# Optimization experiments

Hardware: AMD Instinct MI355X
Metric: run time of the kernel (lower is better)

## Reference

```python
import jax, jax.numpy as jnp
import numpy as np

B, Q, K = 16, 8192, 8192
D_QK, D_V = 64, 64      # raw query/key and value feature dims
H = 8                    # num_heads
DP = 128                 # proj_qks output dim (per default MLP [128, 128])
VP = 64                  # proj_vs output dim (per default MLP [128, 64])
LN_EPS = 1e-6            # flax LayerNorm default


def setup_inputs() -> dict:
    key = jax.random.key(0)
    ks_ = jax.random.split(key, 12)
    f = lambda k, s: jax.random.normal(k, s, jnp.float32)
    return {
        "qs": f(ks_[0], (B, Q, D_QK)),
        "ks": f(ks_[1], (B, K, D_QK)),
        "vs": f(ks_[2], (B, K, D_V)),
        "qs_s": f(ks_[3], (B, Q, D_QK)),
        "ks_s": f(ks_[4], (B, K, D_QK)),
        "valid_lens": jax.random.randint(ks_[5], (B,), 1, K + 1, jnp.int32),
        # proj_qks = MLP([128, 128], gelu): Dense(128) -> gelu -> Dense(128)
        "Wq1": f(ks_[6], (2 * D_QK, DP)) / np.sqrt(2 * D_QK).astype(np.float32),
        "bq1": jnp.zeros((DP,), jnp.float32),
        "Wq2": f(ks_[7], (DP, DP)) / np.sqrt(DP).astype(np.float32),
        "bq2": jnp.zeros((DP,), jnp.float32),
        # proj_vs = MLP([128, 64], gelu): Dense(128) -> gelu -> Dense(64)
        "Wv1": f(ks_[8], (D_V, DP)) / np.sqrt(D_V).astype(np.float32),
        "bv1": jnp.zeros((DP,), jnp.float32),
        "Wv2": f(ks_[9], (DP, VP)) / np.sqrt(DP).astype(np.float32),
        "bv2": jnp.zeros((VP,), jnp.float32),
        "ln_scale": jnp.ones((VP,), jnp.float32),
        "ln_bias": jnp.zeros((VP,), jnp.float32),
    }


def _mlp2(x, W1, b1, W2, b2):
    # Dense -> gelu (tanh approx, flax default) -> Dense
    return jax.nn.gelu(x @ W1 + b1) @ W2 + b2


def reference(qs, ks, vs, qs_s, ks_s, valid_lens,
              Wq1, bq1, Wq2, bq2, Wv1, bv1, Wv2, bv2,
              ln_scale, ln_bias):
    Kl, D = ks.shape[-2], ks.shape[-1]  # D taken BEFORE stacking, as in source
    scale = D ** 0.25
    # stack spatial features then feature-map MLPs
    q = _mlp2(jnp.concatenate([qs_s, qs], axis=-1), Wq1, bq1, Wq2, bq2) / scale
    k = _mlp2(jnp.concatenate([ks_s, ks], axis=-1), Wq1, bq1, Wq2, bq2) / scale
    v = _mlp2(vs, Wv1, bv1, Wv2, bv2)
    # valid-length masking of keys, mean-style normalization of values
    mask = (jnp.arange(Kl)[None, :] < valid_lens[:, None]).astype(k.dtype)[..., None]
    k = k * mask
    v = v / valid_lens[:, None, None].astype(v.dtype)
    Bn, Qn = q.shape[0], q.shape[1]
    q = q.reshape(Bn, Qn, H, DP // H)   # B Q H d
    k = k.reshape(Bn, Kl, H, DP // H)   # B K H d
    v = v.reshape(Bn, Kl, H, VP // H)   # B K H e
    # linear attention: KV outer-product summary then apply queries
    kv = jnp.einsum('bkhd,bkhe->bhde', k, v)          # B H d e
    ctx = jnp.einsum('bqhd,bhde->bqhe', q, kv)        # B Q H e
    ctx = ctx.reshape(Bn, Qn, VP)
    # LayerNorm over last dim
    mu = ctx.mean(-1, keepdims=True)
    var = ((ctx - mu) ** 2).mean(-1, keepdims=True)
    return (ctx - mu) * jax.lax.rsqrt(var + LN_EPS) * ln_scale + ln_bias
```

## Files before the change

### kernel.cpp

```cpp
#include <hip/hip_runtime.h>
#include <hip/hip_bf16.h>


typedef __attribute__((ext_vector_type(8))) short short8;
typedef __attribute__((ext_vector_type(4))) float f32x4;
typedef unsigned int u32;
typedef unsigned short u16;

#define MFMA(A,B,C) __builtin_amdgcn_mfma_f32_16x16x32_bf16((A),(B),(C),0,0,0)
#define SBAR() __builtin_amdgcn_sched_barrier(0)

#define LDH 136
#define LDT 40
#define INVS 0.3535533905932738f

__device__ __forceinline__ u16 bfc(float x){
  __hip_bfloat16 h = __float2bfloat16(x);
  return __bfloat16_as_ushort(h);
}
__device__ __forceinline__ u32 pack2(float a, float b){
  return (u32)bfc(a) | ((u32)bfc(b) << 16);
}
__device__ __forceinline__ float b2f(u16 w){
  return __uint_as_float(((u32)w) << 16);
}
__device__ __forceinline__ short8 cvt8(f32x4 lo, f32x4 hi){
  short8 r;
  r[0]=(short)bfc(lo[0]); r[1]=(short)bfc(lo[1]);
  r[2]=(short)bfc(lo[2]); r[3]=(short)bfc(lo[3]);
  r[4]=(short)bfc(hi[0]); r[5]=(short)bfc(hi[1]);
  r[6]=(short)bfc(hi[2]); r[7]=(short)bfc(hi[3]);
  return r;
}
__device__ __forceinline__ float gelu_f(float x){
  float s = x*x;
  float u = x * __builtin_fmaf(s, 0.035677408136300125f, 0.7978845608028654f);
  float e = __builtin_amdgcn_exp2f(u * -2.885390081777927f);
  return x * __builtin_amdgcn_rcpf(1.0f + e);
}

__global__ void dk_prep(const float* __restrict__ Wq1, const float* __restrict__ Wq2,
                        const float* __restrict__ Wv1, const float* __restrict__ Wv2,
                        u16* __restrict__ wt){
  int i = blockIdx.x*256 + threadIdx.x;
  int e = i & 7;
  int lane = (i >> 3) & 63;
  int chunk = i >> 9;
  int c = lane & 15, g = lane >> 4;
  int k0 = 8*g + e;
  float v;
  if (chunk < 32){
    int mt = chunk >> 2, ks4 = chunk & 3;
    v = Wq1[(ks4*32 + k0)*128 + mt*16 + c];
  } else if (chunk < 64){
    int ch = chunk - 32; int mt = ch >> 2, ks4 = ch & 3;
    v = Wq2[(ks4*32 + k0)*128 + mt*16 + c] * INVS;
  } else if (chunk < 80){
    int ch = chunk - 64; int mt = ch >> 1, ks2 = ch & 1;
    v = Wv1[(ks2*32 + k0)*128 + mt*16 + c];
  } else {
    int ch = chunk - 80; int n2 = ch >> 2, ks4 = ch & 3;
    v = Wv2[(ks4*32 + k0)*64 + n2*16 + c];
  }
  wt[i] = bfc(v);
}

__global__ __launch_bounds__(128, 2) void dk_stage1(
    const float* __restrict__ ksp, const float* __restrict__ kssp,
    const float* __restrict__ vsp, const int* __restrict__ vlen,
    const float* __restrict__ bq1, const float* __restrict__ bq2,
    const float* __restrict__ bv1, const float* __restrict__ bv2,
    const u16* __restrict__ wt, float* __restrict__ kvgr, int repmask)
{
  __shared__ u16 sA[2][5120];
  __shared__ u16 sB[2][2560];
  const int tid = threadIdx.x;
  const int w = tid >> 6, l = tid & 63;
  const int c = l & 15, g = l >> 4;

  int pfx = (l < 16) ? ((vlen[l] + 63) >> 6) : 0;
  #pragma unroll
  for (int m=1; m<16; m<<=1){
    int v = __shfl_up(pfx, m, 64);
    if (l >= m) pfx += v;
  }
  const int T = __shfl(pfx, 15, 64);
  const int t = blockIdx.x;
  if (t >= T) return;
  unsigned long long mk = __ballot(l < 16 && pfx <= t);
  const int b = __popcll(mk);
  const int jb = t - (b ? __shfl(pfx, b-1, 64) : 0);
  const int len = vlen[b];
  const int rbase = jb*64 + w*32;
  if (rbase >= len) return;
  const int rep = t & repmask;
  const size_t row0 = (size_t)b*8192 + rbase;

  u16* H1 = sA[w];
  u16* KT = sA[w];
  u16* VT = sB[w];
  const u16* Wq1t = wt;
  const u16* Wq2t = wt + 16384;
  const u16* Wv1t = wt + 32768;
  const u16* Wv2t = wt + 40960;
  const f32x4 z4 = {0.f,0.f,0.f,0.f};

  {
    f32x4 xvf[8];
    #pragma unroll
    for (int ks2=0; ks2<2; ++ks2){
      #pragma unroll
      for (int nt=0; nt<2; ++nt){
        const float* src = vsp + (row0 + nt*16 + c)*64 + ks2*32 + 8*g;
        xvf[(ks2*2+nt)*2+0] = *(const f32x4*)src;
        xvf[(ks2*2+nt)*2+1] = *(const f32x4*)(src+4);
      }
    }
    SBAR();
    short8 xv[2][2];
    #pragma unroll
    for (int ks2=0; ks2<2; ++ks2)
      #pragma unroll
      for (int nt=0; nt<2; ++nt)
        xv[ks2][nt] = cvt8(xvf[(ks2*2+nt)*2+0], xvf[(ks2*2+nt)*2+1]);
    f32x4 av[8][2];
    #pragma unroll
    for (int mt=0; mt<8; ++mt){ av[mt][0]=z4; av[mt][1]=z4; }
    #pragma unroll
    for (int ks2=0; ks2<2; ++ks2){
      short8 wa[8];
      #pragma unroll
      for (int mt=0; mt<8; ++mt)
        wa[mt] = *(const short8*)&Wv1t[((mt*2+ks2)*64 + l)*8];
      SBAR();
      #pragma unroll
      for (int mt=0; mt<8; ++mt){
        av[mt][0] = MFMA(wa[mt], xv[ks2][0], av[mt][0]);
        av[mt][1] = MFMA(wa[mt], xv[ks2][1], av[mt][1]);
      }
    }
    #pragma unroll
    for (int mt=0; mt<8; ++mt){
      const f32x4 bia = *(const f32x4*)&bv1[mt*16 + 4*g];
      #pragma unroll
      for (int nt=0; nt<2; ++nt){
        uint2 pp;
        pp.x = pack2(gelu_f(av[mt][nt][0]+bia[0]), gelu_f(av[mt][nt][1]+bia[1]));
        pp.y = pack2(gelu_f(av[mt][nt][2]+bia[2]), gelu_f(av[mt][nt][3]+bia[3]));
        *(uint2*)&H1[(nt*16 + c)*LDH + mt*16 + 4*g] = pp;
      }
    }
  }
  {
    f32x4 acv[2][4];
    #pragma unroll
    for (int n2=0; n2<4; ++n2){ acv[0][n2]=z4; acv[1][n2]=z4; }
    #pragma unroll
    for (int ks4=0; ks4<4; ++ks4){
      short8 wb[4];
      #pragma unroll
      for (int n2=0; n2<4; ++n2)
        wb[n2] = *(const short8*)&Wv2t[((n2*4+ks4)*64 + l)*8];
      SBAR();
      const short8 ah0 = *(const short8*)&H1[(c     )*LDH + ks4*32 + 8*g];
      const short8 ah1 = *(const short8*)&H1[(16 + c)*LDH + ks4*32 + 8*g];
      #pragma unroll
      for (int n2=0; n2<4; ++n2){
        acv[0][n2] = MFMA(ah0, wb[n2], acv[0][n2]);
        acv[1][n2] = MFMA(ah1, wb[n2], acv[1][n2]);
      }
    }
    #pragma unroll
    for (int n2=0; n2<4; ++n2){
      const float bb = bv2[n2*16 + c];
      #pragma unroll
      for (int mt=0; mt<2; ++mt){
        uint2 pp;
        pp.x = pack2(acv[mt][n2][0]+bb, acv[mt][n2][1]+bb);
        pp.y = pack2(acv[mt][n2][2]+bb, acv[mt][n2][3]+bb);
        *(uint2*)&VT[(n2*16+c)*LDT + mt*16 + 4*g] = pp;
      }
    }
  }
  {
    f32x4 xkf[16];
    #pragma unroll
    for (int ks4=0; ks4<4; ++ks4){
      #pragma unroll
      for (int nt=0; nt<2; ++nt){
        const int kk = ks4*32 + 8*g;
        const float* src = (ks4 < 2) ? (kssp + (row0 + nt*16 + c)*64 + kk)
                                     : (ksp  + (row0 + nt*16 + c)*64 + (kk - 64));
        xkf[(ks4*2+nt)*2+0] = *(const f32x4*)src;
        xkf[(ks4*2+nt)*2+1] = *(const f32x4*)(src+4);
      }
    }
    SBAR();
    short8 xk[4][2];
    #pragma unroll
    for (int ks4=0; ks4<4; ++ks4)
      #pragma unroll
      for (int nt=0; nt<2; ++nt)
        xk[ks4][nt] = cvt8(xkf[(ks4*2+nt)*2+0], xkf[(ks4*2+nt)*2+1]);
    f32x4 acc[8][2];
    #pragma unroll
    for (int mt=0; mt<8; ++mt){ acc[mt][0]=z4; acc[mt][1]=z4; }
    #pragma unroll
    for (int ks4=0; ks4<4; ++ks4){
      short8 wa[8];
      #pragma unroll
      for (int mt=0; mt<8; ++mt)
        wa[mt] = *(const short8*)&Wq1t[((mt*4+ks4)*64 + l)*8];
      SBAR();
      #pragma unroll
      for (int mt=0; mt<8; ++mt){
        acc[mt][0] = MFMA(wa[mt], xk[ks4][0], acc[mt][0]);
        acc[mt][1] = MFMA(wa[mt], xk[ks4][1], acc[mt][1]);
      }
    }
    #pragma unroll
    for (int mt=0; mt<8; ++mt){
      const f32x4 bia = *(const f32x4*)&bq1[mt*16 + 4*g];
      #pragma unroll
      for (int nt=0; nt<2; ++nt){
        uint2 pp;
        pp.x = pack2(gelu_f(acc[mt][nt][0]+bia[0]), gelu_f(acc[mt][nt][1]+bia[1]));
        pp.y = pack2(gelu_f(acc[mt][nt][2]+bia[2]), gelu_f(acc[mt][nt][3]+bia[3]));
        *(uint2*)&H1[(nt*16 + c)*LDH + mt*16 + 4*g] = pp;
      }
    }
  }
  {
    f32x4 acc2[2][8];
    #pragma unroll
    for (int n2=0; n2<8; ++n2){ acc2[0][n2]=z4; acc2[1][n2]=z4; }
    #pragma unroll
    for (int ks4=0; ks4<4; ++ks4){
      short8 wb[8];
      #pragma unroll
      for (int n2=0; n2<8; ++n2)
        wb[n2] = *(const short8*)&Wq2t[((n2*4+ks4)*64 + l)*8];
      SBAR();
      const short8 ah0 = *(const short8*)&H1[(c     )*LDH + ks4*32 + 8*g];
      const short8 ah1 = *(const short8*)&H1[(16 + c)*LDH + ks4*32 + 8*g];
      #pragma unroll
      for (int n2=0; n2<8; ++n2){
        acc2[0][n2] = MFMA(ah0, wb[n2], acc2[0][n2]);
        acc2[1][n2] = MFMA(ah1, wb[n2], acc2[1][n2]);
      }
    }
    #pragma unroll
    for (int n2=0; n2<8; ++n2){
      const float bb = bq2[n2*16 + c] * INVS;
      #pragma unroll
      for (int mt=0; mt<2; ++mt){
        const int r0 = rbase + mt*16 + 4*g;
        float v0 = (r0+0 < len) ? acc2[mt][n2][0] + bb : 0.f;
        float v1 = (r0+1 < len) ? acc2[mt][n2][1] + bb : 0.f;
        float v2 = (r0+2 < len) ? acc2[mt][n2][2] + bb : 0.f;
        float v3 = (r0+3 < len) ? acc2[mt][n2][3] + bb : 0.f;
        uint2 pp; pp.x = pack2(v0,v1); pp.y = pack2(v2,v3);
        *(uint2*)&KT[(n2*16 + c)*LDT + mt*16 + 4*g] = pp;
      }
    }
  }
  {
    short8 zf = {0,0,0,0,0,0,0,0};
    f32x4 kvacc[8];
    #pragma unroll
    for (int h=0; h<8; ++h) kvacc[h] = z4;
    #pragma unroll
    for (int h=0; h<8; ++h){
      const short8 ka = *(const short8*)&KT[(h*16 + c)*LDT + 8*g];
      short8 vb = zf;
      if (c < 8) vb = *(const short8*)&VT[(h*8 + c)*LDT + 8*g];
      kvacc[h] = MFMA(ka, vb, kvacc[h]);
    }
    if (c < 8){
      float* kvg = kvgr + ((size_t)rep*16 + b)*1024;
      #pragma unroll
      for (int h=0; h<8; ++h){
        #pragma unroll
        for (int r=0; r<4; ++r)
          atomicAdd(&kvg[(h*16 + 4*g + r)*8 + c], kvacc[h][r]);
      }
    }
  }
}

__global__ void dk_mid(const float* __restrict__ kvgr, int nrep,
                       const int* __restrict__ vlen,
                       const float* __restrict__ bq2,
                       const u16* __restrict__ wt,
                       u16* __restrict__ Mt, float* __restrict__ c0g)
{
  __shared__ float kvs[1024];
  const int b = blockIdx.x, t = threadIdx.x;
  const float inv_len = 1.0f / (float)vlen[b];
  #pragma unroll
  for (int k=0; k<4; ++k){
    const int idx = t + 256*k;
    float s = 0.f;
    for (int r=0; r<nrep; ++r) s += kvgr[((size_t)r*16 + b)*1024 + idx];
    kvs[idx] = s * inv_len;
  }
  __syncthreads();
  for (int k=0; k<32; ++k){
    const int o = t + 256*k;
    const int e = o >> 7, j = o & 127;
    const int h = e >> 3, e8 = e & 7;
    const int ks4 = j >> 5, gg = (j >> 3) & 3, el = j & 7;
    float s = 0.f;
    #pragma unroll
    for (int d=0; d<16; ++d){
      const int od = h*16 + d;
      const u16 wv = wt[16384 + (((od>>4)*4 + ks4)*64 + gg*16 + (od&15))*8 + el];
      s += b2f(wv) * kvs[h*128 + d*8 + e8];
    }
    const int n3 = e >> 4, cc = e & 15;
    Mt[(size_t)b*8192 + ((n3*4 + ks4)*64 + gg*16 + cc)*8 + el] = bfc(s);
  }
  if (t < 64){
    const int e = t, h = e >> 3, e8 = e & 7;
    float s = 0.f;
    #pragma unroll
    for (int d=0; d<16; ++d)
      s += bq2[h*16+d] * INVS * kvs[h*128 + d*8 + e8];
    c0g[b*64 + e] = s;
  }
}

__global__ __launch_bounds__(128, 2) void dk_stage2(
    const float* __restrict__ qsp, const float* __restrict__ qssp,
    const float* __restrict__ bq1,
    const float* __restrict__ lnw_g, const float* __restrict__ lnb_g,
    const u16* __restrict__ wt, const u16* __restrict__ Mt,
    const float* __restrict__ c0g, float* __restrict__ outp)
{
  __shared__ u16 sH1[2][32*LDH];
  const int tid = threadIdx.x;
  const int w = tid >> 6, l = tid & 63;
  const int c = l & 15, g = l >> 4;
  const int b  = blockIdx.x >> 7;
  const int jb = blockIdx.x & 127;
  const int rbase = jb*64 + w*32;
  u16* H1 = sH1[w];
  const u16* Wq1t = wt;
  const size_t row0 = (size_t)b*8192 + rbase;
  const f32x4 z4 = {0.f,0.f,0.f,0.f};

  {
    f32x4 xqf[16];
    #pragma unroll
    for (int ks4=0; ks4<4; ++ks4){
      #pragma unroll
      for (int nt=0; nt<2; ++nt){
        const int kk = ks4*32 + 8*g;
        const float* src = (ks4 < 2) ? (qssp + (row0 + nt*16 + c)*64 + kk)
                                     : (qsp  + (row0 + nt*16 + c)*64 + (kk - 64));
        xqf[(ks4*2+nt)*2+0] = *(const f32x4*)src;
        xqf[(ks4*2+nt)*2+1] = *(const f32x4*)(src+4);
      }
    }
    SBAR();
    short8 xq[4][2];
    #pragma unroll
    for (int ks4=0; ks4<4; ++ks4)
      #pragma unroll
      for (int nt=0; nt<2; ++nt)
        xq[ks4][nt] = cvt8(xqf[(ks4*2+nt)*2+0], xqf[(ks4*2+nt)*2+1]);
    f32x4 acc[8][2];
    #pragma unroll
    for (int mt=0; mt<8; ++mt){ acc[mt][0]=z4; acc[mt][1]=z4; }
    #pragma unroll
    for (int ks4=0; ks4<4; ++ks4){
      short8 wa[8];
      #pragma unroll
      for (int mt=0; mt<8; ++mt)
        wa[mt] = *(const short8*)&Wq1t[((mt*4+ks4)*64 + l)*8];
      SBAR();
      #pragma unroll
      for (int mt=0; mt<8; ++mt){
        acc[mt][0] = MFMA(wa[mt], xq[ks4][0], acc[mt][0]);
        acc[mt][1] = MFMA(wa[mt], xq[ks4][1], acc[mt][1]);
      }
    }
    #pragma unroll
    for (int mt=0; mt<8; ++mt){
      const f32x4 bia = *(const f32x4*)&bq1[mt*16 + 4*g];
      #pragma unroll
      for (int nt=0; nt<2; ++nt){
        uint2 pp;
        pp.x = pack2(gelu_f(acc[mt][nt][0]+bia[0]), gelu_f(acc[mt][nt][1]+bia[1]));
        pp.y = pack2(gelu_f(acc[mt][nt][2]+bia[2]), gelu_f(acc[mt][nt][3]+bia[3]));
        *(uint2*)&H1[(nt*16 + c)*LDH + mt*16 + 4*g] = pp;
      }
    }
  }
  f32x4 acc3[2][4];
  #pragma unroll
  for (int n3=0; n3<4; ++n3){ acc3[0][n3]=z4; acc3[1][n3]=z4; }
  const u16* Mb = Mt + (size_t)b*8192;
  {
    short8 bm[16];
    #pragma unroll
    for (int ks4=0; ks4<4; ++ks4)
      #pragma unroll
      for (int n3=0; n3<4; ++n3)
        bm[ks4*4+n3] = *(const short8*)&Mb[((n3*4+ks4)*64 + l)*8];
    SBAR();
    #pragma unroll
    for (int ks4=0; ks4<4; ++ks4){
      const short8 aq0 = *(const short8*)&H1[(c     )*LDH + ks4*32 + 8*g];
      const short8 aq1 = *(const short8*)&H1[(16 + c)*LDH + ks4*32 + 8*g];
      #pragma unroll
      for (int n3=0; n3<4; ++n3){
        acc3[0][n3] = MFMA(aq0, bm[ks4*4+n3], acc3[0][n3]);
        acc3[1][n3] = MFMA(aq1, bm[ks4*4+n3], acc3[1][n3]);
      }
    }
  }
  float c0v[4];
  #pragma unroll
  for (int n3=0; n3<4; ++n3) c0v[n3] = c0g[b*64 + n3*16 + c];
  float lnw[4], lnb[4];
  #pragma unroll
  for (int n3=0; n3<4; ++n3){ lnw[n3] = lnw_g[n3*16 + c]; lnb[n3] = lnb_g[n3*16 + c]; }
  float* Tb = (float*)H1;
  #pragma unroll
  for (int mt=0; mt<2; ++mt){
    #pragma unroll
    for (int r=0; r<4; ++r){
      float s1 = 0.f, s2 = 0.f;
      #pragma unroll
      for (int n3=0; n3<4; ++n3){
        float v = acc3[mt][n3][r] + c0v[n3];
        s1 += v; s2 += v*v;
      }
      #pragma unroll
      for (int m=1; m<16; m<<=1){
        s1 += __shfl_xor(s1, m, 64);
        s2 += __shfl_xor(s2, m, 64);
      }
      const float mu = s1 * (1.0f/64.0f);
      const float var = s2 * (1.0f/64.0f) - mu*mu;
      const float rs = rsqrtf(var + 1e-6f);
      const int rloc = mt*16 + 4*g + r;
      #pragma unroll
      for (int n3=0; n3<4; ++n3)
        Tb[rloc*68 + n3*16 + c] = (acc3[mt][n3][r] + c0v[n3] - mu)*rs*lnw[n3] + lnb[n3];
    }
  }
  float* ob = outp + row0*64;
  #pragma unroll
  for (int i=0; i<8; ++i){
    const int row = i*4 + (l>>4);
    const f32x4 vv = *(const f32x4*)&Tb[row*68 + (l&15)*4];
    *(f32x4*)(ob + row*64 + (l&15)*4) = vv;
  }
}

extern "C" void kernel_launch(void* const* d_in, const int* in_sizes, int n_in,
                              void* d_out, int out_size, void* d_ws, size_t ws_size,
                              hipStream_t stream)
{
  const float* qs   = (const float*)d_in[0];
  const float* ks   = (const float*)d_in[1];
  const float* vs   = (const float*)d_in[2];
  const float* qs_s = (const float*)d_in[3];
  const float* ks_s = (const float*)d_in[4];
  const int*   vl   = (const int*)d_in[5];
  const float* Wq1  = (const float*)d_in[6];
  const float* bq1  = (const float*)d_in[7];
  const float* Wq2  = (const float*)d_in[8];
  const float* bq2  = (const float*)d_in[9];
  const float* Wv1  = (const float*)d_in[10];
  const float* bv1  = (const float*)d_in[11];
  const float* Wv2  = (const float*)d_in[12];
  const float* bv2  = (const float*)d_in[13];
  const float* lnw  = (const float*)d_in[14];
  const float* lnb  = (const float*)d_in[15];
  (void)in_sizes; (void)n_in; (void)out_size;

  const size_t fixed = 96*1024 + 256*1024 + 4096;
  int nrep = 4;
  while (nrep > 1 && (size_t)nrep*65536 + fixed > ws_size) nrep >>= 1;
  float* kvgr = (float*)d_ws;
  u16*   wt   = (u16*)((char*)d_ws + (size_t)nrep*65536);
  u16*   Mt   = (u16*)((char*)wt + 96*1024);
  float* c0   = (float*)((char*)Mt + 256*1024);

  hipMemsetAsync(kvgr, 0, (size_t)nrep*65536, stream);
  dk_prep<<<192, 256, 0, stream>>>(Wq1, Wq2, Wv1, Wv2, wt);
  dk_stage1<<<2048, 128, 0, stream>>>(ks, ks_s, vs, vl, bq1, bq2, bv1, bv2,
                                      wt, kvgr, nrep - 1);
  dk_mid<<<16, 256, 0, stream>>>(kvgr, nrep, vl, bq2, wt, Mt, c0);
  dk_stage2<<<2048, 128, 0, stream>>>(qs, qs_s, bq1, lnw, lnb, wt, Mt, c0,
                                      (float*)d_out);
}
```

Baseline: 92.17 us.

## Halve rows per wave to 16 and double grid with higher occupancy

Each wave now processes 16 rows instead of 32 in both stage kernels, halving accumulator arrays, input register buffers and LDS buffers, while doubling the grid to 4096 blocks and raising launch bounds to 4 blocks per SIMD. The KV outer-product MFMA now uses a K-dimension of 16 by zeroing the upper lane groups. The aim is more resident waves to hide global-load latency. In exchange, each weight fragment loaded from global/L2 is reused over half as many rows, so weight traffic per row doubles, and half the KV MFMA work is wasted on zeros.

```diff
diff --git a/kernel.cpp b/kernel.cpp
--- a/kernel.cpp
+++ b/kernel.cpp
@@ -11,7 +11,7 @@
 #define SBAR() __builtin_amdgcn_sched_barrier(0)
 
 #define LDH 136
-#define LDT 40
+#define LDT 24
 #define INVS 0.3535533905932738f
 
 __device__ __forceinline__ u16 bfc(float x){
@@ -65,20 +65,20 @@
   wt[i] = bfc(v);
 }
 
-__global__ __launch_bounds__(128, 2) void dk_stage1(
+__global__ __launch_bounds__(128, 4) void dk_stage1(
     const float* __restrict__ ksp, const float* __restrict__ kssp,
     const float* __restrict__ vsp, const int* __restrict__ vlen,
     const float* __restrict__ bq1, const float* __restrict__ bq2,
     const float* __restrict__ bv1, const float* __restrict__ bv2,
     const u16* __restrict__ wt, float* __restrict__ kvgr, int repmask)
 {
-  __shared__ u16 sA[2][5120];
-  __shared__ u16 sB[2][2560];
+  __shared__ u16 sA[2][3072];
+  __shared__ u16 sB[2][1536];
   const int tid = threadIdx.x;
   const int w = tid >> 6, l = tid & 63;
   const int c = l & 15, g = l >> 4;
 
-  int pfx = (l < 16) ? ((vlen[l] + 63) >> 6) : 0;
+  int pfx = (l < 16) ? ((vlen[l] + 31) >> 5) : 0;
   #pragma unroll
   for (int m=1; m<16; m<<=1){
     int v = __shfl_up(pfx, m, 64);
@@ -91,7 +91,7 @@
   const int b = __popcll(mk);
   const int jb = t - (b ? __shfl(pfx, b-1, 64) : 0);
   const int len = vlen[b];
-  const int rbase = jb*64 + w*32;
+  const int rbase = jb*32 + w*16;
   if (rbase >= len) return;
   const int rep = t & repmask;
   const size_t row0 = (size_t)b*8192 + rbase;
@@ -104,28 +104,24 @@
   const u16* Wv1t = wt + 32768;
   const u16* Wv2t = wt + 40960;
   const f32x4 z4 = {0.f,0.f,0.f,0.f};
-
-  {
-    f32x4 xvf[8];
+  const short8 zf = {0,0,0,0,0,0,0,0};
+
+  {
+    f32x4 xvf[4];
     #pragma unroll
     for (int ks2=0; ks2<2; ++ks2){
-      #pragma unroll
-      for (int nt=0; nt<2; ++nt){
-        const float* src = vsp + (row0 + nt*16 + c)*64 + ks2*32 + 8*g;
-        xvf[(ks2*2+nt)*2+0] = *(const f32x4*)src;
-        xvf[(ks2*2+nt)*2+1] = *(const f32x4*)(src+4);
-      }
+      const float* src = vsp + (row0 + c)*64 + ks2*32 + 8*g;
+      xvf[ks2*2+0] = *(const f32x4*)src;
+      xvf[ks2*2+1] = *(const f32x4*)(src+4);
     }
     SBAR();
-    short8 xv[2][2];
+    short8 xv[2];
     #pragma unroll
     for (int ks2=0; ks2<2; ++ks2)
-      #pragma unroll
-      for (int nt=0; nt<2; ++nt)
-        xv[ks2][nt] = cvt8(xvf[(ks2*2+nt)*2+0], xvf[(ks2*2+nt)*2+1]);
-    f32x4 av[8][2];
-    #pragma unroll
-    for (int mt=0; mt<8; ++mt){ av[mt][0]=z4; av[mt][1]=z4; }
+      xv[ks2] = cvt8(xvf[ks2*2+0], xvf[ks2*2+1]);
+    f32x4 av[8];
+    #pragma unroll
+    for (int mt=0; mt<8; ++mt) av[mt] = z4;
     #pragma unroll
     for (int ks2=0; ks2<2; ++ks2){
       short8 wa[8];
@@ -134,27 +130,22 @@
         wa[mt] = *(const short8*)&Wv1t[((mt*2+ks2)*64 + l)*8];
       SBAR();
       #pragma unroll
-      for (int mt=0; mt<8; ++mt){
-        av[mt][0] = MFMA(wa[mt], xv[ks2][0], av[mt][0]);
-        av[mt][1] = MFMA(wa[mt], xv[ks2][1], av[mt][1]);
-      }
+      for (int mt=0; mt<8; ++mt)
+        av[mt] = MFMA(wa[mt], xv[ks2], av[mt]);
     }
     #pragma unroll
     for (int mt=0; mt<8; ++mt){
       const f32x4 bia = *(const f32x4*)&bv1[mt*16 + 4*g];
-      #pragma unroll
-      for (int nt=0; nt<2; ++nt){
-        uint2 pp;
-        pp.x = pack2(gelu_f(av[mt][nt][0]+bia[0]), gelu_f(av[mt][nt][1]+bia[1]));
-        pp.y = pack2(gelu_f(av[mt][nt][2]+bia[2]), gelu_f(av[mt][nt][3]+bia[3]));
-        *(uint2*)&H1[(nt*16 + c)*LDH + mt*16 + 4*g] = pp;
-      }
-    }
-  }
-  {
-    f32x4 acv[2][4];
-    #pragma unroll
-    for (int n2=0; n2<4; ++n2){ acv[0][n2]=z4; acv[1][n2]=z4; }
+      uint2 pp;
+      pp.x = pack2(gelu_f(av[mt][0]+bia[0]), gelu_f(av[mt][1]+bia[1]));
+      pp.y = pack2(gelu_f(av[mt][2]+bia[2]), gelu_f(av[mt][3]+bia[3]));
+      *(uint2*)&H1[c*LDH + mt*16 + 4*g] = pp;
+    }
+  }
+  {
+    f32x4 acv[4];
+    #pragma unroll
+    for (int n2=0; n2<4; ++n2) acv[n2] = z4;
     #pragma unroll
     for (int ks4=0; ks4<4; ++ks4){
       short8 wb[4];
@@ -162,49 +153,38 @@
       for (int n2=0; n2<4; ++n2)
         wb[n2] = *(const short8*)&Wv2t[((n2*4+ks4)*64 + l)*8];
       SBAR();
-      const short8 ah0 = *(const short8*)&H1[(c     )*LDH + ks4*32 + 8*g];
-      const short8 ah1 = *(const short8*)&H1[(16 + c)*LDH + ks4*32 + 8*g];
-      #pragma unroll
-      for (int n2=0; n2<4; ++n2){
-        acv[0][n2] = MFMA(ah0, wb[n2], acv[0][n2]);
-        acv[1][n2] = MFMA(ah1, wb[n2], acv[1][n2]);
-      }
+      const short8 ah = *(const short8*)&H1[c*LDH + ks4*32 + 8*g];
+      #pragma unroll
+      for (int n2=0; n2<4; ++n2)
+        acv[n2] = MFMA(ah, wb[n2], acv[n2]);
     }
     #pragma unroll
     for (int n2=0; n2<4; ++n2){
       const float bb = bv2[n2*16 + c];
-      #pragma unroll
-      for (int mt=0; mt<2; ++mt){
-        uint2 pp;
-        pp.x = pack2(acv[mt][n2][0]+bb, acv[mt][n2][1]+bb);
-        pp.y = pack2(acv[mt][n2][2]+bb, acv[mt][n2][3]+bb);
-        *(uint2*)&VT[(n2*16+c)*LDT + mt*16 + 4*g] = pp;
-      }
-    }
-  }
-  {
-    f32x4 xkf[16];
-    #pragma unroll
-    for (int ks4=0; ks4<4; ++ks4){
-      #pragma unroll
-      for (int nt=0; nt<2; ++nt){
-        const int kk = ks4*32 + 8*g;
-        const float* src = (ks4 < 2) ? (kssp + (row0 + nt*16 + c)*64 + kk)
-                                     : (ksp  + (row0 + nt*16 + c)*64 + (kk - 64));
-        xkf[(ks4*2+nt)*2+0] = *(const f32x4*)src;
-        xkf[(ks4*2+nt)*2+1] = *(const f32x4*)(src+4);
-      }
+      uint2 pp;
+      pp.x = pack2(acv[n2][0]+bb, acv[n2][1]+bb);
+      pp.y = pack2(acv[n2][2]+bb, acv[n2][3]+bb);
+      *(uint2*)&VT[(n2*16+c)*LDT + 4*g] = pp;
+    }
+  }
+  {
+    f32x4 xkf[8];
+    #pragma unroll
+    for (int ks4=0; ks4<4; ++ks4){
+      const int kk = ks4*32 + 8*g;
+      const float* src = (ks4 < 2) ? (kssp + (row0 + c)*64 + kk)
+                                   : (ksp  + (row0 + c)*64 + (kk - 64));
+      xkf[ks4*2+0] = *(const f32x4*)src;
+      xkf[ks4*2+1] = *(const f32x4*)(src+4);
     }
     SBAR();
-    short8 xk[4][2];
+    short8 xk[4];
     #pragma unroll
     for (int ks4=0; ks4<4; ++ks4)
-      #pragma unroll
-      for (int nt=0; nt<2; ++nt)
-        xk[ks4][nt] = cvt8(xkf[(ks4*2+nt)*2+0], xkf[(ks4*2+nt)*2+1]);
-    f32x4 acc[8][2];
-    #pragma unroll
-    for (int mt=0; mt<8; ++mt){ acc[mt][0]=z4; acc[mt][1]=z4; }
+      xk[ks4] = cvt8(xkf[ks4*2+0], xkf[ks4*2+1]);
+    f32x4 acc[8];
+    #pragma unroll
+    for (int mt=0; mt<8; ++mt) acc[mt] = z4;
     #pragma unroll
     for (int ks4=0; ks4<4; ++ks4){
       short8 wa[8];
@@ -213,27 +193,22 @@
         wa[mt] = *(const short8*)&Wq1t[((mt*4+ks4)*64 + l)*8];
       SBAR();
       #pragma unroll
-      for (int mt=0; mt<8; ++mt){
-        acc[mt][0] = MFMA(wa[mt], xk[ks4][0], acc[mt][0]);
-        acc[mt][1] = MFMA(wa[mt], xk[ks4][1], acc[mt][1]);
-      }
+      for (int mt=0; mt<8; ++mt)
+        acc[mt] = MFMA(wa[mt], xk[ks4], acc[mt]);
     }
     #pragma unroll
     for (int mt=0; mt<8; ++mt){
       const f32x4 bia = *(const f32x4*)&bq1[mt*16 + 4*g];
-      #pragma unroll
-      for (int nt=0; nt<2; ++nt){
-        uint2 pp;
-        pp.x = pack2(gelu_f(acc[mt][nt][0]+bia[0]), gelu_f(acc[mt][nt][1]+bia[1]));
-        pp.y = pack2(gelu_f(acc[mt][nt][2]+bia[2]), gelu_f(acc[mt][nt][3]+bia[3]));
-        *(uint2*)&H1[(nt*16 + c)*LDH + mt*16 + 4*g] = pp;
-      }
-    }
-  }
-  {
-    f32x4 acc2[2][8];
-    #pragma unroll
-    for (int n2=0; n2<8; ++n2){ acc2[0][n2]=z4; acc2[1][n2]=z4; }
+      uint2 pp;
+      pp.x = pack2(gelu_f(acc[mt][0]+bia[0]), gelu_f(acc[mt][1]+bia[1]));
+      pp.y = pack2(gelu_f(acc[mt][2]+bia[2]), gelu_f(acc[mt][3]+bia[3]));
+      *(uint2*)&H1[c*LDH + mt*16 + 4*g] = pp;
+    }
+  }
+  {
+    f32x4 acc2[8];
+    #pragma unroll
+    for (int n2=0; n2<8; ++n2) acc2[n2] = z4;
     #pragma unroll
     for (int ks4=0; ks4<4; ++ks4){
       short8 wb[8];
@@ -241,39 +216,33 @@
       for (int n2=0; n2<8; ++n2)
         wb[n2] = *(const short8*)&Wq2t[((n2*4+ks4)*64 + l)*8];
       SBAR();
-      const short8 ah0 = *(const short8*)&H1[(c     )*LDH + ks4*32 + 8*g];
-      const short8 ah1 = *(const short8*)&H1[(16 + c)*LDH + ks4*32 + 8*g];
-      #pragma unroll
-      for (int n2=0; n2<8; ++n2){
-        acc2[0][n2] = MFMA(ah0, wb[n2], acc2[0][n2]);
-        acc2[1][n2] = MFMA(ah1, wb[n2], acc2[1][n2]);
-      }
+      const short8 ah = *(const short8*)&H1[c*LDH + ks4*32 + 8*g];
+      #pragma unroll
+      for (int n2=0; n2<8; ++n2)
+        acc2[n2] = MFMA(ah, wb[n2], acc2[n2]);
     }
     #pragma unroll
     for (int n2=0; n2<8; ++n2){
       const float bb = bq2[n2*16 + c] * INVS;
-      #pragma unroll
-      for (int mt=0; mt<2; ++mt){
-        const int r0 = rbase + mt*16 + 4*g;
-        float v0 = (r0+0 < len) ? acc2[mt][n2][0] + bb : 0.f;
-        float v1 = (r0+1 < len) ? acc2[mt][n2][1] + bb : 0.f;
-        float v2 = (r0+2 < len) ? acc2[mt][n2][2] + bb : 0.f;
-        float v3 = (r0+3 < len) ? acc2[mt][n2][3] + bb : 0.f;
-        uint2 pp; pp.x = pack2(v0,v1); pp.y = pack2(v2,v3);
-        *(uint2*)&KT[(n2*16 + c)*LDT + mt*16 + 4*g] = pp;
-      }
-    }
-  }
-  {
-    short8 zf = {0,0,0,0,0,0,0,0};
+      const int r0 = rbase + 4*g;
+      float v0 = (r0+0 < len) ? acc2[n2][0] + bb : 0.f;
+      float v1 = (r0+1 < len) ? acc2[n2][1] + bb : 0.f;
+      float v2 = (r0+2 < len) ? acc2[n2][2] + bb : 0.f;
+      float v3 = (r0+3 < len) ? acc2[n2][3] + bb : 0.f;
+      uint2 pp; pp.x = pack2(v0,v1); pp.y = pack2(v2,v3);
+      *(uint2*)&KT[(n2*16 + c)*LDT + 4*g] = pp;
+    }
+  }
+  {
     f32x4 kvacc[8];
     #pragma unroll
     for (int h=0; h<8; ++h) kvacc[h] = z4;
     #pragma unroll
     for (int h=0; h<8; ++h){
-      const short8 ka = *(const short8*)&KT[(h*16 + c)*LDT + 8*g];
-      short8 vb = zf;
-      if (c < 8) vb = *(const short8*)&VT[(h*8 + c)*LDT + 8*g];
+      const short8 kaL = *(const short8*)&KT[(h*16 + c)*LDT + 8*(g&1)];
+      const short8 vbL = *(const short8*)&VT[(h*8 + (c&7))*LDT + 8*(g&1)];
+      const short8 ka = (g < 2) ? kaL : zf;
+      const short8 vb = (c < 8 && g < 2) ? vbL : zf;
       kvacc[h] = MFMA(ka, vb, kvacc[h]);
     }
     if (c < 8){
@@ -330,48 +299,44 @@
   }
 }
 
-__global__ __launch_bounds__(128, 2) void dk_stage2(
+__global__ __launch_bounds__(128, 4) void dk_stage2(
     const float* __restrict__ qsp, const float* __restrict__ qssp,
     const float* __restrict__ bq1,
     const float* __restrict__ lnw_g, const float* __restrict__ lnb_g,
     const u16* __restrict__ wt, const u16* __restrict__ Mt,
     const float* __restrict__ c0g, float* __restrict__ outp)
 {
-  __shared__ u16 sH1[2][32*LDH];
+  __shared__ u16 sH1[2][2176];
   const int tid = threadIdx.x;
   const int w = tid >> 6, l = tid & 63;
   const int c = l & 15, g = l >> 4;
-  const int b  = blockIdx.x >> 7;
-  const int jb = blockIdx.x & 127;
-  const int rbase = jb*64 + w*32;
+  const int b  = blockIdx.x >> 8;
+  const int jb = blockIdx.x & 255;
+  const int rbase = jb*32 + w*16;
   u16* H1 = sH1[w];
   const u16* Wq1t = wt;
   const size_t row0 = (size_t)b*8192 + rbase;
   const f32x4 z4 = {0.f,0.f,0.f,0.f};
-
-  {
-    f32x4 xqf[16];
-    #pragma unroll
-    for (int ks4=0; ks4<4; ++ks4){
-      #pragma unroll
-      for (int nt=0; nt<2; ++nt){
-        const int kk = ks4*32 + 8*g;
-        const float* src = (ks4 < 2) ? (qssp + (row0 + nt*16 + c)*64 + kk)
-                                     : (qsp  + (row0 + nt*16 + c)*64 + (kk - 64));
-        xqf[(ks4*2+nt)*2+0] = *(const f32x4*)src;
-        xqf[(ks4*2+nt)*2+1] = *(const f32x4*)(src+4);
-      }
+  const u16* Mb = Mt + (size_t)b*8192;
+
+  {
+    f32x4 xqf[8];
+    #pragma unroll
+    for (int ks4=0; ks4<4; ++ks4){
+      const int kk = ks4*32 + 8*g;
+      const float* src = (ks4 < 2) ? (qssp + (row0 + c)*64 + kk)
+                                   : (qsp  + (row0 + c)*64 + (kk - 64));
+      xqf[ks4*2+0] = *(const f32x4*)src;
+      xqf[ks4*2+1] = *(const f32x4*)(src+4);
     }
     SBAR();
-    short8 xq[4][2];
+    short8 xq[4];
     #pragma unroll
     for (int ks4=0; ks4<4; ++ks4)
-      #pragma unroll
-      for (int nt=0; nt<2; ++nt)
-        xq[ks4][nt] = cvt8(xqf[(ks4*2+nt)*2+0], xqf[(ks4*2+nt)*2+1]);
-    f32x4 acc[8][2];
-    #pragma unroll
-    for (int mt=0; mt<8; ++mt){ acc[mt][0]=z4; acc[mt][1]=z4; }
+      xq[ks4] = cvt8(xqf[ks4*2+0], xqf[ks4*2+1]);
+    f32x4 acc[8];
+    #pragma unroll
+    for (int mt=0; mt<8; ++mt) acc[mt] = z4;
     #pragma unroll
     for (int ks4=0; ks4<4; ++ks4){
       short8 wa[8];
@@ -380,27 +345,21 @@
         wa[mt] = *(const short8*)&Wq1t[((mt*4+ks4)*64 + l)*8];
       SBAR();
       #pragma unroll
-      for (int mt=0; mt<8; ++mt){
-        acc[mt][0] = MFMA(wa[mt], xq[ks4][0], acc[mt][0]);
-        acc[mt][1] = MFMA(wa[mt], xq[ks4][1], acc[mt][1]);
-      }
+      for (int mt=0; mt<8; ++mt)
+        acc[mt] = MFMA(wa[mt], xq[ks4], acc[mt]);
     }
     #pragma unroll
     for (int mt=0; mt<8; ++mt){
       const f32x4 bia = *(const f32x4*)&bq1[mt*16 + 4*g];
-      #pragma unroll
-      for (int nt=0; nt<2; ++nt){
-        uint2 pp;
-        pp.x = pack2(gelu_f(acc[mt][nt][0]+bia[0]), gelu_f(acc[mt][nt][1]+bia[1]));
-        pp.y = pack2(gelu_f(acc[mt][nt][2]+bia[2]), gelu_f(acc[mt][nt][3]+bia[3]));
-        *(uint2*)&H1[(nt*16 + c)*LDH + mt*16 + 4*g] = pp;
-      }
-    }
-  }
-  f32x4 acc3[2][4];
-  #pragma unroll
-  for (int n3=0; n3<4; ++n3){ acc3[0][n3]=z4; acc3[1][n3]=z4; }
-  const u16* Mb = Mt + (size_t)b*8192;
+      uint2 pp;
+      pp.x = pack2(gelu_f(acc[mt][0]+bia[0]), gelu_f(acc[mt][1]+bia[1]));
+      pp.y = pack2(gelu_f(acc[mt][2]+bia[2]), gelu_f(acc[mt][3]+bia[3]));
+      *(uint2*)&H1[c*LDH + mt*16 + 4*g] = pp;
+    }
+  }
+  f32x4 acc3[4];
+  #pragma unroll
+  for (int n3=0; n3<4; ++n3) acc3[n3] = z4;
   {
     short8 bm[16];
     #pragma unroll
@@ -411,13 +370,10 @@
     SBAR();
     #pragma unroll
     for (int ks4=0; ks4<4; ++ks4){
-      const short8 aq0 = *(const short8*)&H1[(c     )*LDH + ks4*32 + 8*g];
-      const short8 aq1 = *(const short8*)&H1[(16 + c)*LDH + ks4*32 + 8*g];
-      #pragma unroll
-      for (int n3=0; n3<4; ++n3){
-        acc3[0][n3] = MFMA(aq0, bm[ks4*4+n3], acc3[0][n3]);
-        acc3[1][n3] = MFMA(aq1, bm[ks4*4+n3], acc3[1][n3]);
-      }
+      const short8 aq = *(const short8*)&H1[c*LDH + ks4*32 + 8*g];
+      #pragma unroll
+      for (int n3=0; n3<4; ++n3)
+        acc3[n3] = MFMA(aq, bm[ks4*4+n3], acc3[n3]);
     }
   }
   float c0v[4];
@@ -428,32 +384,29 @@
   for (int n3=0; n3<4; ++n3){ lnw[n3] = lnw_g[n3*16 + c]; lnb[n3] = lnb_g[n3*16 + c]; }
   float* Tb = (float*)H1;
   #pragma unroll
-  for (int mt=0; mt<2; ++mt){
-    #pragma unroll
-    for (int r=0; r<4; ++r){
-      float s1 = 0.f, s2 = 0.f;
-      #pragma unroll
-      for (int n3=0; n3<4; ++n3){
-        float v = acc3[mt][n3][r] + c0v[n3];
-        s1 += v; s2 += v*v;
-      }
-      #pragma unroll
-      for (int m=1; m<16; m<<=1){
-        s1 += __shfl_xor(s1, m, 64);
-        s2 += __shfl_xor(s2, m, 64);
-      }
-      const float mu = s1 * (1.0f/64.0f);
-      const float var = s2 * (1.0f/64.0f) - mu*mu;
-      const float rs = rsqrtf(var + 1e-6f);
-      const int rloc = mt*16 + 4*g + r;
-      #pragma unroll
-      for (int n3=0; n3<4; ++n3)
-        Tb[rloc*68 + n3*16 + c] = (acc3[mt][n3][r] + c0v[n3] - mu)*rs*lnw[n3] + lnb[n3];
-    }
+  for (int r=0; r<4; ++r){
+    float s1 = 0.f, s2 = 0.f;
+    #pragma unroll
+    for (int n3=0; n3<4; ++n3){
+      float v = acc3[n3][r] + c0v[n3];
+      s1 += v; s2 += v*v;
+    }
+    #pragma unroll
+    for (int m=1; m<16; m<<=1){
+      s1 += __shfl_xor(s1, m, 64);
+      s2 += __shfl_xor(s2, m, 64);
+    }
+    const float mu = s1 * (1.0f/64.0f);
+    const float var = s2 * (1.0f/64.0f) - mu*mu;
+    const float rs = rsqrtf(var + 1e-6f);
+    const int rloc = 4*g + r;
+    #pragma unroll
+    for (int n3=0; n3<4; ++n3)
+      Tb[rloc*68 + n3*16 + c] = (acc3[n3][r] + c0v[n3] - mu)*rs*lnw[n3] + lnb[n3];
   }
   float* ob = outp + row0*64;
   #pragma unroll
-  for (int i=0; i<8; ++i){
+  for (int i=0; i<4; ++i){
     const int row = i*4 + (l>>4);
     const f32x4 vv = *(const f32x4*)&Tb[row*68 + (l&15)*4];
     *(f32x4*)(ob + row*64 + (l&15)*4) = vv;
@@ -492,9 +445,9 @@
 
   hipMemsetAsync(kvgr, 0, (size_t)nrep*65536, stream);
   dk_prep<<<192, 256, 0, stream>>>(Wq1, Wq2, Wv1, Wv2, wt);
-  dk_stage1<<<2048, 128, 0, stream>>>(ks, ks_s, vs, vl, bq1, bq2, bv1, bv2,
+  dk_stage1<<<4096, 128, 0, stream>>>(ks, ks_s, vs, vl, bq1, bq2, bv1, bv2,
                                       wt, kvgr, nrep - 1);
   dk_mid<<<16, 256, 0, stream>>>(kvgr, nrep, vl, bq2, wt, Mt, c0);
-  dk_stage2<<<2048, 128, 0, stream>>>(qs, qs_s, bq1, lnw, lnb, wt, Mt, c0,
+  dk_stage2<<<4096, 128, 0, stream>>>(qs, qs_s, bq1, lnw, lnb, wt, Mt, c0,
                                       (float*)d_out);
 }
```

Result: slower. 117.7 us (+27.7%).
